# Kernel optimization log

Measured on AMD Instinct MI355X. Metric: run time of the kernel, lower is better.

## Reference

```python
import jax, jax.numpy as jnp
from jax import lax
import numpy as np

HEADS = 4
BUCKET = 64
DEPTH = 4


def _conv(x, w, b):
    y = lax.conv_general_dilated(x, w, (1, 1), [(1, 1), (1, 1)],
                                 dimension_numbers=('NCHW', 'OIHW', 'NCHW'))
    return y + b[None, :, None, None]


def _convT(x, w, b):
    # torch ConvTranspose2d(k=4, s=2, p=1): flip kernel, swap io, lhs_dilation=2, pad k-1-p=2
    wk = jnp.flip(w, (2, 3)).transpose(1, 0, 2, 3)
    y = lax.conv_general_dilated(x, wk, (1, 1), [(2, 2), (2, 2)], lhs_dilation=(2, 2),
                                 dimension_numbers=('NCHW', 'OIHW', 'NCHW'))
    return y + b[None, :, None, None]


def _maxpool(x):
    return lax.reduce_window(x, -jnp.inf, lax.max, (1, 1, 2, 2), (1, 1, 2, 2), 'VALID')


def _ln(x, g, b):
    m = x.mean(-1, keepdims=True)
    v = ((x - m) ** 2).mean(-1, keepdims=True)
    return (x - m) / jnp.sqrt(v + 1e-5) * g + b


def _lsh_attention(x, Wqk, bqk, Wv, bv, Wo, bo, rot):
    # shared-QK LSH bucketed attention (single hash round), look-one-back chunks
    B, N, D = x.shape
    h, dh = HEADS, D // HEADS
    qk = (x @ Wqk + bqk).reshape(B, N, h, dh).transpose(0, 2, 1, 3)  # B h N dh
    v = (x @ Wv + bv).reshape(B, N, h, dh).transpose(0, 2, 1, 3)
    k = qk / (jnp.linalg.norm(qk, axis=-1, keepdims=True) + 1e-6)    # keys = normalized queries
    rotated = jnp.einsum('bhnd,hdr->bhnr', qk, rot)
    buckets = jnp.argmax(jnp.concatenate([rotated, -rotated], -1), -1)  # B h N
    ticker = jnp.arange(N)
    perm = jnp.argsort(buckets * N + ticker, axis=-1)  # stable sort by bucket
    inv_perm = jnp.argsort(perm, axis=-1)
    g = lambda t: jnp.take_along_axis(t, perm[..., None], axis=2)
    nc = N // BUCKET
    bq = g(qk).reshape(B, h, nc, BUCKET, dh)
    bk = g(k).reshape(B, h, nc, BUCKET, dh)
    bv_ = g(v).reshape(B, h, nc, BUCKET, dh)
    bk2 = jnp.concatenate([bk, jnp.roll(bk, 1, axis=2)], axis=3)   # look one chunk back
    bv2 = jnp.concatenate([bv_, jnp.roll(bv_, 1, axis=2)], axis=3)
    dots = jnp.einsum('bhcid,bhcjd->bhcij', bq, bk2) * (dh ** -0.5)
    spos = jnp.take_along_axis(jnp.broadcast_to(ticker, buckets.shape), perm, -1).reshape(B, h, nc, BUCKET)
    kpos = jnp.concatenate([spos, jnp.roll(spos, 1, axis=2)], axis=3)
    dots = jnp.where(spos[..., :, None] == kpos[..., None, :], -1e5, dots)  # mask self (q == k)
    attn = jax.nn.softmax(dots, -1)
    o = jnp.einsum('bhcij,bhcjd->bhcid', attn, bv2).reshape(B, h, N, dh)
    o = jnp.take_along_axis(o, inv_perm[..., None], axis=2)  # unsort
    return o.transpose(0, 2, 1, 3).reshape(B, N, D) @ Wo + bo


def _reformer(seq, ln1_g, ln1_b, Wqk, bqk, Wv, bv, Wo, bo, rot, ln2_g, ln2_b, Wff1, bff1, Wff2, bff2):
    for i in range(DEPTH):
        seq = seq + _lsh_attention(_ln(seq, ln1_g[i], ln1_b[i]), Wqk[i], bqk[i], Wv[i], bv[i], Wo[i], bo[i], rot[i])
        hdn = jax.nn.gelu(_ln(seq, ln2_g[i], ln2_b[i]) @ Wff1[i] + bff1[i])
        seq = seq + hdn @ Wff2[i] + bff2[i]
    return seq


def _forward(burst, conv1_w, conv1_b, conv2_w, conv2_b, conv3_w, conv3_b,
             ln1_g, ln1_b, Wqk, bqk, Wv, bv, Wo, bo, rot, ln2_g, ln2_b,
             Wff1, bff1, Wff2, bff2, up1_w, up1_b, dec1_w, dec1_b,
             up2_w, up2_b, dec2_w, dec2_b, out_w, out_b):
    B, T, C, H, W = burst.shape
    x = burst.reshape(B * T, C, H, W)
    e1 = jax.nn.relu(_conv(x, conv1_w, conv1_b))
    p1 = _maxpool(e1)
    e2 = jax.nn.relu(_conv(p1, conv2_w, conv2_b))
    p2 = _maxpool(e2)
    bm = jax.nn.relu(_conv(p2, conv3_w, conv3_b))
    D = bm.shape[1]
    Hq, Wq = H // 4, W // 4
    seq = bm.transpose(0, 2, 3, 1).reshape(B * T, Hq * Wq, D)
    seq = _reformer(seq, ln1_g, ln1_b, Wqk, bqk, Wv, bv, Wo, bo, rot, ln2_g, ln2_b, Wff1, bff1, Wff2, bff2)
    bm = seq.reshape(B * T, Hq, Wq, D).transpose(0, 3, 1, 2)
    d1 = _convT(bm, up1_w, up1_b)
    d1 = jax.nn.relu(_conv(jnp.concatenate([d1, e2], 1), dec1_w, dec1_b))
    d2 = _convT(d1, up2_w, up2_b)
    d2 = jax.nn.relu(_conv(jnp.concatenate([d2, e1], 1), dec2_w, dec2_b))
    sharp = jax.nn.sigmoid(_conv(d2, out_w, out_b))
    return sharp.reshape(B, T, C, H, W)[:, 0]


def setup_inputs() -> dict:
    key = jax.random.key(0)
    ks = jax.random.split(key, 20)
    s = 0.05
    n = lambda k, shape: jax.random.normal(k, shape, jnp.float32) * s
    inp = {}
    inp['burst'] = jax.random.uniform(ks[0], (1, 7, 3, 256, 256), jnp.float32)
    inp['conv1_w'] = n(ks[1], (64, 3, 3, 3)); inp['conv1_b'] = jnp.zeros((64,), jnp.float32)
    inp['conv2_w'] = n(ks[2], (128, 64, 3, 3)); inp['conv2_b'] = jnp.zeros((128,), jnp.float32)
    inp['conv3_w'] = n(ks[3], (256, 128, 3, 3)); inp['conv3_b'] = jnp.zeros((256,), jnp.float32)
    inp['ln1_g'] = jnp.ones((4, 256), jnp.float32); inp['ln1_b'] = jnp.zeros((4, 256), jnp.float32)
    inp['Wqk'] = n(ks[4], (4, 256, 256)); inp['bqk'] = jnp.zeros((4, 256), jnp.float32)
    inp['Wv'] = n(ks[5], (4, 256, 256)); inp['bv'] = jnp.zeros((4, 256), jnp.float32)
    inp['Wo'] = n(ks[6], (4, 256, 256)); inp['bo'] = jnp.zeros((4, 256), jnp.float32)
    inp['rot'] = jax.random.normal(ks[7], (4, 4, 64, 32), jnp.float32)  # depth, heads, d_head, n_buckets//2
    inp['ln2_g'] = jnp.ones((4, 256), jnp.float32); inp['ln2_b'] = jnp.zeros((4, 256), jnp.float32)
    inp['Wff1'] = n(ks[8], (4, 256, 1024)); inp['bff1'] = jnp.zeros((4, 1024), jnp.float32)
    inp['Wff2'] = n(ks[9], (4, 1024, 256)); inp['bff2'] = jnp.zeros((4, 256), jnp.float32)
    inp['up1_w'] = n(ks[10], (256, 128, 4, 4)); inp['up1_b'] = jnp.zeros((128,), jnp.float32)
    inp['dec1_w'] = n(ks[11], (128, 256, 3, 3)); inp['dec1_b'] = jnp.zeros((128,), jnp.float32)
    inp['up2_w'] = n(ks[12], (128, 64, 4, 4)); inp['up2_b'] = jnp.zeros((64,), jnp.float32)
    inp['dec2_w'] = n(ks[13], (64, 128, 3, 3)); inp['dec2_b'] = jnp.zeros((64,), jnp.float32)
    inp['out_w'] = n(ks[14], (3, 64, 3, 3)); inp['out_b'] = jnp.zeros((3,), jnp.float32)
    return inp


def reference(burst, conv1_w, conv1_b, conv2_w, conv2_b, conv3_w, conv3_b,
              ln1_g, ln1_b, Wqk, bqk, Wv, bv, Wo, bo, rot, ln2_g, ln2_b,
              Wff1, bff1, Wff2, bff2, up1_w, up1_b, dec1_w, dec1_b,
              up2_w, up2_b, dec2_w, dec2_b, out_w, out_b):
    return _forward(burst, conv1_w, conv1_b, conv2_w, conv2_b, conv3_w, conv3_b,
                    ln1_g, ln1_b, Wqk, bqk, Wv, bv, Wo, bo, rot, ln2_g, ln2_b,
                    Wff1, bff1, Wff2, bff2, up1_w, up1_b, dec1_w, dec1_b,
                    up2_w, up2_b, dec2_w, dec2_b, out_w, out_b)
```

## Files before the change

kernel.cpp:

```cpp
#include <hip/hip_runtime.h>
#include <hip/hip_bf16.h>
#include <math.h>

using short8  = __attribute__((ext_vector_type(8))) short;
using half8   = __attribute__((ext_vector_type(8))) _Float16;
using floatx4 = __attribute__((ext_vector_type(4))) float;

static __device__ __forceinline__ float gelu_f(float x) {
    float x3 = x * x * x;
    return 0.5f * x * (1.f + tanhf(0.7978845608028654f * (x + 0.044715f * x3)));
}
static __device__ __forceinline__ short f2h(float f) {
    _Float16 h = (_Float16)f;
    return __builtin_bit_cast(short, h);
}
static __device__ __forceinline__ short f2bf(float f) {
    unsigned u = __float_as_uint(f);
    u += 0x7fffu + ((u >> 16) & 1u);
    return (short)(u >> 16);
}
static __device__ __forceinline__ float bf2f(short s) {
    return __uint_as_float(((unsigned)(unsigned short)s) << 16);
}
struct bf3s { short a, b, c; };
static __device__ __forceinline__ bf3s split3(float v) {
    short c0 = f2bf(v); float r = v - bf2f(c0);
    short c1 = f2bf(r); r -= bf2f(c1);
    short c2 = f2bf(r);
    bf3s s; s.a = c0; s.b = c1; s.c = c2; return s;
}

template <int OCB>
__global__ __launch_bounds__(256) void conv1_nhwc_kernel(
    const float* __restrict__ in1, const float* __restrict__ w,
    const float* __restrict__ bias, float* __restrict__ out, int H, int W, int OC)
{
    int tx = threadIdx.x, ty = threadIdx.y;
    int x = blockIdx.x * 16 + tx, y = blockIdx.y * 16 + ty;
    int oc0 = blockIdx.z * OCB;
    const int C = 3;
    float acc[OCB];
#pragma unroll
    for (int o = 0; o < OCB; ++o) acc[o] = 0.f;
    for (int ic = 0; ic < C; ++ic) {
        const float* src = in1 + (size_t)ic * H * W;
        float v[9];
#pragma unroll
        for (int ky = 0; ky < 3; ++ky) {
            int iy = y + ky - 1;
            bool okY = (iy >= 0) && (iy < H);
#pragma unroll
            for (int kx = 0; kx < 3; ++kx) {
                int ix = x + kx - 1;
                bool ok = okY && (ix >= 0) && (ix < W);
                v[ky * 3 + kx] = ok ? src[(size_t)iy * W + ix] : 0.f;
            }
        }
        const float* wp = w + ((size_t)oc0 * C + ic) * 9;
#pragma unroll
        for (int o = 0; o < OCB; ++o) {
            const float* wo = wp + (size_t)o * C * 9;
            acc[o] += v[0]*wo[0] + v[1]*wo[1] + v[2]*wo[2]
                    + v[3]*wo[3] + v[4]*wo[4] + v[5]*wo[5]
                    + v[6]*wo[6] + v[7]*wo[7] + v[8]*wo[8];
        }
    }
    float* op = out + ((size_t)y * W + x) * OC + oc0;
#pragma unroll
    for (int o = 0; o < OCB; ++o)
        op[o] = fmaxf(acc[o] + bias[oc0 + o], 0.f);
}

__global__ __launch_bounds__(256) void maxpool1_bf3_kernel(
    const float* __restrict__ in, short* __restrict__ o0, short* __restrict__ o1,
    short* __restrict__ o2, int OW, int IW, int C)
{
    int idx = blockIdx.x * 256 + threadIdx.x;
    int g = idx % (C >> 2); int p = idx / (C >> 2);
    int x = p % OW; int y = p / OW;
    size_t base = ((size_t)(2 * y) * IW + 2 * x) * C + g * 4;
    float4 a = *(const float4*)(in + base);
    float4 b = *(const float4*)(in + base + C);
    float4 c = *(const float4*)(in + base + (size_t)IW * C);
    float4 d = *(const float4*)(in + base + (size_t)IW * C + C);
    float v[4];
    v[0] = fmaxf(fmaxf(a.x, b.x), fmaxf(c.x, d.x));
    v[1] = fmaxf(fmaxf(a.y, b.y), fmaxf(c.y, d.y));
    v[2] = fmaxf(fmaxf(a.z, b.z), fmaxf(c.z, d.z));
    v[3] = fmaxf(fmaxf(a.w, b.w), fmaxf(c.w, d.w));
    size_t o = (size_t)p * C + g * 4;
#pragma unroll
    for (int j = 0; j < 4; ++j) {
        bf3s s = split3(v[j]);
        o0[o + j] = s.a; o1[o + j] = s.b; o2[o + j] = s.c;
    }
}

__global__ __launch_bounds__(256) void maxpool2_bf3_kernel(
    const short* __restrict__ i0, const short* __restrict__ i1,
    const short* __restrict__ i2, short* __restrict__ o0, short* __restrict__ o1,
    short* __restrict__ o2, int OW, int IW, int C)
{
    int idx = blockIdx.x * 256 + threadIdx.x;
    int g = idx % (C >> 2); int p = idx / (C >> 2);
    int x = p % OW; int y = p / OW;
    float v[4] = {-1e30f, -1e30f, -1e30f, -1e30f};
#pragma unroll
    for (int dy = 0; dy < 2; ++dy)
#pragma unroll
        for (int dx = 0; dx < 2; ++dx) {
            size_t base = ((size_t)(2 * y + dy) * IW + 2 * x + dx) * C + g * 4;
#pragma unroll
            for (int j = 0; j < 4; ++j) {
                float u = bf2f(i0[base + j]) + bf2f(i1[base + j]) + bf2f(i2[base + j]);
                v[j] = fmaxf(v[j], u);
            }
        }
    size_t o = (size_t)p * C + g * 4;
#pragma unroll
    for (int j = 0; j < 4; ++j) {
        bf3s s = split3(v[j]);
        o0[o + j] = s.a; o1[o + j] = s.b; o2[o + j] = s.c;
    }
}

__global__ void pack_conv3_kernel(const float* __restrict__ w,
                                  short* __restrict__ B0, short* __restrict__ B1,
                                  short* __restrict__ B2, int C, int OC, int total)
{
    int t = blockIdx.x * 256 + threadIdx.x;
    if (t >= total) return;
    int lane = t & 63, fi = t >> 6;
    int NT = OC >> 4;
    int nt = fi % NT, kt = fi / NT;
    int cpt = C >> 5;
    int tap = kt / cpt, ct = kt % cpt;
    int c = ct * 32 + (lane >> 4) * 8;
    int oc = nt * 16 + (lane & 15);
    short8 v0, v1, v2;
#pragma unroll
    for (int j = 0; j < 8; ++j) {
        bf3s s = split3(w[((size_t)oc * C + c + j) * 9 + tap]);
        v0[j] = s.a; v1[j] = s.b; v2[j] = s.c;
    }
    ((short8*)B0)[t] = v0; ((short8*)B1)[t] = v1; ((short8*)B2)[t] = v2;
}

__global__ __launch_bounds__(256) void conv_bf3_kernel(
    const short* __restrict__ ia0, const short* __restrict__ ia1,
    const short* __restrict__ ia2,
    const short* __restrict__ B0, const short* __restrict__ B1,
    const short* __restrict__ B2, const float* __restrict__ bias,
    float* __restrict__ outf, short* __restrict__ o0, short* __restrict__ o1,
    short* __restrict__ o2, short* __restrict__ oh,
    int H, int W, int C, int OC)
{
    int tid = threadIdx.x, wave = tid >> 6, lane = tid & 63;
    int quad = lane >> 4, l16 = lane & 15;
    int x0 = blockIdx.x * 64, y = blockIdx.y, nt0 = blockIdx.z * 4;
    int cpt = C >> 5, NT = OC >> 4;
    const short8* b0p = (const short8*)B0;
    const short8* b1p = (const short8*)B1;
    const short8* b2p = (const short8*)B2;
    floatx4 aM[4] = {{0,0,0,0},{0,0,0,0},{0,0,0,0},{0,0,0,0}};
    floatx4 aC[4] = {{0,0,0,0},{0,0,0,0},{0,0,0,0},{0,0,0,0}};
    int xm = x0 + wave * 16 + l16;
    for (int ky = 0; ky < 3; ++ky) {
        int yy = y + ky - 1;
        bool rok = (yy >= 0) && (yy < H);
        for (int kx = 0; kx < 3; ++kx) {
            int xx = xm + kx - 1;
            bool ok = rok && (xx >= 0) && (xx < W);
            size_t pos = (size_t)yy * W + xx;
            int ktb = (ky * 3 + kx) * cpt;
            for (int ct = 0; ct < cpt; ++ct) {
                int cc = ct * 32 + quad * 8;
                short8 A0 = {0,0,0,0,0,0,0,0}, A1 = A0, A2 = A0;
                if (ok) {
                    A0 = *(const short8*)(ia0 + pos * C + cc);
                    A1 = *(const short8*)(ia1 + pos * C + cc);
                    A2 = *(const short8*)(ia2 + pos * C + cc);
                }
                size_t bi = ((size_t)(ktb + ct) * NT + nt0) * 64 + lane;
#pragma unroll
                for (int s = 0; s < 4; ++s) {
                    short8 w0 = b0p[bi + s * 64];
                    short8 w1 = b1p[bi + s * 64];
                    short8 w2 = b2p[bi + s * 64];
                    aM[s] = __builtin_amdgcn_mfma_f32_16x16x32_bf16(A0, w0, aM[s], 0, 0, 0);
                    aC[s] = __builtin_amdgcn_mfma_f32_16x16x32_bf16(A0, w1, aC[s], 0, 0, 0);
                    aC[s] = __builtin_amdgcn_mfma_f32_16x16x32_bf16(A1, w0, aC[s], 0, 0, 0);
                    aC[s] = __builtin_amdgcn_mfma_f32_16x16x32_bf16(A0, w2, aC[s], 0, 0, 0);
                    aC[s] = __builtin_amdgcn_mfma_f32_16x16x32_bf16(A1, w1, aC[s], 0, 0, 0);
                    aC[s] = __builtin_amdgcn_mfma_f32_16x16x32_bf16(A2, w0, aC[s], 0, 0, 0);
                }
            }
        }
    }
#pragma unroll
    for (int s = 0; s < 4; ++s) {
        int n = (nt0 + s) * 16 + l16;
        float bs = bias[n];
#pragma unroll
        for (int r = 0; r < 4; ++r) {
            int m = wave * 16 + quad * 4 + r;
            int x = x0 + m;
            float v = fmaxf(aM[s][r] + aC[s][r] + bs, 0.f);
            size_t o = ((size_t)y * W + x) * OC + n;
            if (outf) outf[o] = v;
            else {
                bf3s sp = split3(v);
                o0[o] = sp.a; o1[o] = sp.b; o2[o] = sp.c;
                oh[o] = f2h(v);
            }
        }
    }
}

__global__ __launch_bounds__(256) void ln_bf3_kernel(
    const float* __restrict__ x, const float* __restrict__ g,
    const float* __restrict__ b, short* __restrict__ y0,
    short* __restrict__ y1, short* __restrict__ y2)
{
    int wave = threadIdx.x >> 6, lane = threadIdx.x & 63;
    int n = blockIdx.x * 4 + wave;
    const float* xr = x + (size_t)n * 256;
    float4 v = *(const float4*)(xr + lane * 4);
    float s = v.x + v.y + v.z + v.w;
#pragma unroll
    for (int m = 1; m < 64; m <<= 1) s += __shfl_xor(s, m);
    float mean = s * (1.f / 256.f);
    float cx = v.x - mean, cy = v.y - mean, cz = v.z - mean, cw = v.w - mean;
    float q = cx * cx + cy * cy + cz * cz + cw * cw;
#pragma unroll
    for (int m = 1; m < 64; m <<= 1) q += __shfl_xor(q, m);
    float rstd = rsqrtf(q * (1.f / 256.f) + 1e-5f);
    float4 gv = *(const float4*)(g + lane * 4);
    float4 bv = *(const float4*)(b + lane * 4);
    float o[4];
    o[0] = cx * rstd * gv.x + bv.x;
    o[1] = cy * rstd * gv.y + bv.y;
    o[2] = cz * rstd * gv.z + bv.z;
    o[3] = cw * rstd * gv.w + bv.w;
    size_t ob = (size_t)n * 256 + lane * 4;
#pragma unroll
    for (int j = 0; j < 4; ++j) {
        bf3s sp = split3(o[j]);
        y0[ob + j] = sp.a; y1[ob + j] = sp.b; y2[ob + j] = sp.c;
    }
}

__global__ __launch_bounds__(256) void knorm_kernel(
    const float* __restrict__ qk, float* __restrict__ knrm)
{
    int t = blockIdx.x * 256 + threadIdx.x;
    int h = t >> 12, n = t & 4095;
    const float* q = qk + (size_t)n * 256 + h * 64;
    float s = 0.f;
#pragma unroll
    for (int d = 0; d < 64; d += 4) {
        float4 v = *(const float4*)(q + d);
        s += v.x * v.x + v.y * v.y + v.z * v.z + v.w * v.w;
    }
    knrm[t] = 1.f / (sqrtf(s) + 1e-6f);
}

__global__ __launch_bounds__(256) void bucket_kernel(
    const float* __restrict__ qk, const float* __restrict__ rot,
    int* __restrict__ buckets)
{
    int t = blockIdx.x * 256 + threadIdx.x;
    int h = t >> 12, n = t & 4095;
    const float* q = qk + (size_t)n * 256 + h * 64;
    const float* R = rot + (size_t)h * 2048;
    float acc[32];
#pragma unroll
    for (int r = 0; r < 32; ++r) acc[r] = 0.f;
    for (int d = 0; d < 64; ++d) {
        float qd = q[d];
        const float* Rd = R + d * 32;
#pragma unroll
        for (int r = 0; r < 32; ++r) acc[r] += qd * Rd[r];
    }
    float bvv = acc[0]; int best = 0;
#pragma unroll
    for (int j = 1; j < 64; ++j) {
        float val = (j < 32) ? acc[j] : -acc[j - 32];
        if (val > bvv) { bvv = val; best = j; }
    }
    buckets[t] = best;
}

__global__ __launch_bounds__(256) void lsh_sort_kernel(
    const int* __restrict__ buckets, int* __restrict__ perm)
{
    int h = blockIdx.x;
    const int* bk = buckets + h * 4096;
    __shared__ unsigned long long mask[64][64];
    __shared__ int counts[64];
    __shared__ int offsets[64];
    __shared__ int wpre[64][64];
    int tid = threadIdx.x, wave = tid >> 6, lane = tid & 63;
    for (int w = wave * 16; w < wave * 16 + 16; ++w) {
        int bl = bk[w * 64 + lane];
        for (int b = 0; b < 64; ++b) {
            unsigned long long m = __ballot(bl == b);
            if (lane == b) mask[b][w] = m;
        }
    }
    __syncthreads();
    if (tid < 64) {
        int c = 0;
        for (int w = 0; w < 64; ++w) c += __popcll(mask[tid][w]);
        counts[tid] = c;
    }
    __syncthreads();
    if (tid == 0) {
        int a = 0;
        for (int b = 0; b < 64; ++b) { offsets[b] = a; a += counts[b]; }
    }
    __syncthreads();
    for (int b = wave * 16; b < wave * 16 + 16; ++b) {
        int c = __popcll(mask[b][lane]);
        int incl = c;
#pragma unroll
        for (int off = 1; off < 64; off <<= 1) {
            int nb = __shfl_up(incl, off);
            if (lane >= off) incl += nb;
        }
        wpre[b][lane] = incl - c + offsets[b];
    }
    __syncthreads();
    for (int i = tid; i < 4096; i += 256) {
        int b = bk[i]; int w = i >> 6; int l = i & 63;
        unsigned long long below = mask[b][w] & ((1ull << l) - 1ull);
        int pos = wpre[b][w] + __popcll(below);
        perm[h * 4096 + pos] = i;
    }
}

__global__ __launch_bounds__(256) void attn_kernel(
    const float* __restrict__ qk, const float* __restrict__ vv,
    const float* __restrict__ knrm, const int* __restrict__ perm,
    short* __restrict__ o0, short* __restrict__ o1, short* __restrict__ o2)
{
    __shared__ float ks[128 * 64];
    __shared__ float dotsT[128 * 64];
    int c = blockIdx.x, h = blockIdx.y;
    int tid = threadIdx.x;
    const int* pm = perm + h * 4096;
    int cm = (c + 63) & 63;
    {
        int jr = tid >> 1, hf = tid & 1;
        int sk = (jr < 64) ? (c * 64 + jr) : (cm * 64 + (jr - 64));
        int nk = pm[sk];
        float sc = knrm[h * 4096 + nk];
        const float* src = qk + (size_t)nk * 256 + h * 64 + hf * 32;
        float* dst = ks + jr * 64 + hf * 32;
#pragma unroll
        for (int d = 0; d < 32; d += 4) {
            float4 v = *(const float4*)(src + d);
            v.x *= sc; v.y *= sc; v.z *= sc; v.w *= sc;
            *(float4*)(dst + d) = v;
        }
    }
    __syncthreads();
    int r = tid & 63, jg = tid >> 6;
    int nq = pm[c * 64 + r];
    {
        float qreg[64];
        const float* src = qk + (size_t)nq * 256 + h * 64;
#pragma unroll
        for (int d = 0; d < 64; d += 4) {
            float4 v = *(const float4*)(src + d);
            qreg[d] = v.x; qreg[d + 1] = v.y; qreg[d + 2] = v.z; qreg[d + 3] = v.w;
        }
        for (int j = jg * 32; j < jg * 32 + 32; ++j) {
            const float* kr = ks + j * 64;
            float dot = 0.f;
#pragma unroll
            for (int d = 0; d < 64; ++d) dot += qreg[d] * kr[d];
            int sk = (j < 64) ? (c * 64 + j) : (cm * 64 + (j - 64));
            int nk = pm[sk];
            dot = (nk == nq) ? -1e5f : dot * 0.125f;
            dotsT[j * 64 + r] = dot;
        }
    }
    __syncthreads();
    {
        int jr = tid >> 1, hf = tid & 1;
        int sk = (jr < 64) ? (c * 64 + jr) : (cm * 64 + (jr - 64));
        int nk = pm[sk];
        const float* src = vv + (size_t)nk * 256 + h * 64 + hf * 32;
        float* dst = ks + jr * 64 + hf * 32;
#pragma unroll
        for (int d = 0; d < 32; d += 4)
            *(float4*)(dst + d) = *(const float4*)(src + d);
    }
    if (tid < 64) {
        int rr = tid;
        float mx = -1e30f;
        for (int j = 0; j < 128; ++j) mx = fmaxf(mx, dotsT[j * 64 + rr]);
        float s = 0.f;
        for (int j = 0; j < 128; ++j) {
            float e = expf(dotsT[j * 64 + rr] - mx);
            dotsT[j * 64 + rr] = e; s += e;
        }
        float inv = 1.f / s;
        for (int j = 0; j < 128; ++j) dotsT[j * 64 + rr] *= inv;
    }
    __syncthreads();
    int dg = jg;
    float acc[16];
#pragma unroll
    for (int d = 0; d < 16; ++d) acc[d] = 0.f;
    for (int j = 0; j < 128; ++j) {
        float a = dotsT[j * 64 + r];
        const float* vr = ks + j * 64 + dg * 16;
#pragma unroll
        for (int d = 0; d < 16; ++d) acc[d] += a * vr[d];
    }
    size_t ob = (size_t)nq * 256 + h * 64 + dg * 16;
#pragma unroll
    for (int d = 0; d < 16; ++d) {
        bf3s sp = split3(acc[d]);
        o0[ob + d] = sp.a; o1[ob + d] = sp.b; o2[ob + d] = sp.c;
    }
}

static __device__ __forceinline__ void pack_one(
    const float* __restrict__ W, short* __restrict__ B0, short* __restrict__ B1,
    short* __restrict__ B2, int N, int t)
{
    int lane = t & 63, fi = t >> 6;
    int NT = N >> 4;
    int nt = fi % NT, kt = fi / NT;
    int n = nt * 16 + (lane & 15);
    int k0 = kt * 32 + (lane >> 4) * 8;
    short8 v0, v1, v2;
#pragma unroll
    for (int j = 0; j < 8; ++j) {
        bf3s s = split3(W[(size_t)(k0 + j) * N + n]);
        v0[j] = s.a; v1[j] = s.b; v2[j] = s.c;
    }
    ((short8*)B0)[t] = v0; ((short8*)B1)[t] = v1; ((short8*)B2)[t] = v2;
}

__global__ void pack_layer_kernel(
    const float* __restrict__ Wqk, const float* __restrict__ Wv,
    const float* __restrict__ Wo, const float* __restrict__ Wff1,
    const float* __restrict__ Wff2,
    short* q0, short* q1, short* q2, short* v0, short* v1, short* v2,
    short* o0, short* o1, short* o2, short* f10, short* f11, short* f12,
    short* f20, short* f21, short* f22)
{
    int t = blockIdx.x * 256 + threadIdx.x;
    if (t < 8192)       pack_one(Wqk, q0, q1, q2, 256, t);
    else if (t < 16384) pack_one(Wv, v0, v1, v2, 256, t - 8192);
    else if (t < 24576) pack_one(Wo, o0, o1, o2, 256, t - 16384);
    else if (t < 57344) pack_one(Wff1, f10, f11, f12, 1024, t - 24576);
    else if (t < 90112) pack_one(Wff2, f20, f21, f22, 256, t - 57344);
}

static __device__ __forceinline__ void gemm_bf3_core(
    const short* __restrict__ A0, const short* __restrict__ A1,
    const short* __restrict__ A2,
    const short* __restrict__ B0, const short* __restrict__ B1,
    const short* __restrict__ B2, const float* __restrict__ bias,
    float* __restrict__ Cf, short* __restrict__ D0, short* __restrict__ D1,
    short* __restrict__ D2, int N, int K, int act, int resid, int bx, int by)
{
    int tid = threadIdx.x, wave = tid >> 6, lane = tid & 63;
    int quad = lane >> 4, l16 = lane & 15;
    int m0 = by * 64 + wave * 16;
    int NT = N >> 4, nt0 = bx * 4;
    size_t arow = (size_t)(m0 + l16) * K + quad * 8;
    const short8* b0p = (const short8*)B0;
    const short8* b1p = (const short8*)B1;
    const short8* b2p = (const short8*)B2;
    floatx4 aM[4] = {{0,0,0,0},{0,0,0,0},{0,0,0,0},{0,0,0,0}};
    floatx4 aC[4] = {{0,0,0,0},{0,0,0,0},{0,0,0,0},{0,0,0,0}};
    int KT = K >> 5;
    for (int kt = 0; kt < KT; ++kt) {
        short8 a0 = *(const short8*)(A0 + arow + kt * 32);
        short8 a1 = *(const short8*)(A1 + arow + kt * 32);
        short8 a2 = *(const short8*)(A2 + arow + kt * 32);
        size_t bi = ((size_t)kt * NT + nt0) * 64 + lane;
#pragma unroll
        for (int s = 0; s < 4; ++s) {
            short8 w0 = b0p[bi + s * 64];
            short8 w1 = b1p[bi + s * 64];
            short8 w2 = b2p[bi + s * 64];
            aM[s] = __builtin_amdgcn_mfma_f32_16x16x32_bf16(a0, w0, aM[s], 0, 0, 0);
            aC[s] = __builtin_amdgcn_mfma_f32_16x16x32_bf16(a0, w1, aC[s], 0, 0, 0);
            aC[s] = __builtin_amdgcn_mfma_f32_16x16x32_bf16(a1, w0, aC[s], 0, 0, 0);
            aC[s] = __builtin_amdgcn_mfma_f32_16x16x32_bf16(a0, w2, aC[s], 0, 0, 0);
            aC[s] = __builtin_amdgcn_mfma_f32_16x16x32_bf16(a1, w1, aC[s], 0, 0, 0);
            aC[s] = __builtin_amdgcn_mfma_f32_16x16x32_bf16(a2, w0, aC[s], 0, 0, 0);
        }
    }
#pragma unroll
    for (int s = 0; s < 4; ++s) {
        int n = (nt0 + s) * 16 + l16;
        float bs = bias[n];
#pragma unroll
        for (int r = 0; r < 4; ++r) {
            int m = m0 + quad * 4 + r;
            float v = aM[s][r] + aC[s][r] + bs;
            if (act == 1) v = gelu_f(v);
            size_t o = (size_t)m * N + n;
            if (D0) {
                bf3s sp = split3(v);
                D0[o] = sp.a; D1[o] = sp.b; D2[o] = sp.c;
            } else {
                if (resid) v += Cf[o];
                Cf[o] = v;
            }
        }
    }
}

__global__ __launch_bounds__(256) void gemm_bf3_kernel(
    const short* A0, const short* A1, const short* A2,
    const short* B0, const short* B1, const short* B2,
    const float* bias, float* Cf, short* D0, short* D1, short* D2,
    int N, int K, int act, int resid)
{
    gemm_bf3_core(A0, A1, A2, B0, B1, B2, bias, Cf, D0, D1, D2,
                  N, K, act, resid, blockIdx.x, blockIdx.y);
}

__global__ __launch_bounds__(256) void gemm_qkv_bf3_kernel(
    const short* A0, const short* A1, const short* A2,
    const short* Q0, const short* Q1, const short* Q2,
    const float* qb, float* Cq,
    const short* V0, const short* V1, const short* V2,
    const float* vb, float* Cv, int K)
{
    int side = blockIdx.x >> 2;
    gemm_bf3_core(A0, A1, A2, side ? V0 : Q0, side ? V1 : Q1, side ? V2 : Q2,
                  side ? vb : qb, side ? Cv : Cq, nullptr, nullptr, nullptr,
                  256, K, 0, 0, blockIdx.x & 3, blockIdx.y);
}

__global__ void pack_conv_kernel(const float* __restrict__ w, short* __restrict__ Bp,
                                 int C, int OC, int NT, int total)
{
    int t = blockIdx.x * 256 + threadIdx.x;
    if (t >= total) return;
    int lane = t & 63, fi = t >> 6;
    int nt = fi % NT, kt = fi / NT;
    int cpt = C >> 5;
    int tap = kt / cpt, ct = kt % cpt;
    int c = ct * 32 + (lane >> 4) * 8;
    int oc = nt * 16 + (lane & 15);
    short8 v;
#pragma unroll
    for (int j = 0; j < 8; ++j) {
        float f = (oc < OC) ? w[((size_t)oc * C + c + j) * 9 + tap] : 0.f;
        v[j] = f2h(f);
    }
    ((short8*)Bp)[t] = v;
}

__global__ void pack_convt_kernel(const float* __restrict__ w, short* __restrict__ Bp,
                                  int IC, int OC, int total)
{
    int t = blockIdx.x * 256 + threadIdx.x;
    if (t >= total) return;
    int lane = t & 63, fi = t >> 6;
    int NT = OC >> 4, cpt = IC >> 5, KT4 = 4 * cpt;
    int nt = fi % NT, r = fi / NT;
    int kt = r % KT4, pz = r / KT4;
    int py = pz >> 1, px = pz & 1;
    int t4 = kt / cpt, ct = kt % cpt;
    int ty = t4 >> 1, tx = t4 & 1;
    int ky = py ? (2 * ty) : (1 + 2 * ty);
    int kx = px ? (2 * tx) : (1 + 2 * tx);
    int ic = ct * 32 + (lane >> 4) * 8;
    int oc = nt * 16 + (lane & 15);
    short8 v;
#pragma unroll
    for (int j = 0; j < 8; ++j)
        v[j] = f2h(w[(((size_t)(ic + j) * OC + oc) * 4 + ky) * 4 + kx]);
    ((short8*)Bp)[t] = v;
}

__global__ __launch_bounds__(256) void conv_mfma_kernel(
    const short* __restrict__ in1, int C1, const short* __restrict__ in2, int C2,
    const short* __restrict__ Bp, const float* __restrict__ bias,
    short* __restrict__ outb, int H, int W, int OC)
{
    int tid = threadIdx.x, wave = tid >> 6, lane = tid & 63;
    int quad = lane >> 4, l16 = lane & 15;
    int x0 = blockIdx.x * 64, y = blockIdx.y, nt0 = blockIdx.z * 4;
    int C = C1 + C2, cpt = C >> 5, NT = OC >> 4;
    const half8* bp = (const half8*)Bp;
    floatx4 acc[4] = {{0,0,0,0},{0,0,0,0},{0,0,0,0},{0,0,0,0}};
    int xm = x0 + wave * 16 + l16;
    for (int ky = 0; ky < 3; ++ky) {
        int yy = y + ky - 1;
        bool rok = (yy >= 0) && (yy < H);
        for (int kx = 0; kx < 3; ++kx) {
            int xx = xm + kx - 1;
            bool ok = rok && (xx >= 0) && (xx < W);
            size_t pos = (size_t)yy * W + xx;
            int ktb = (ky * 3 + kx) * cpt;
            for (int ct = 0; ct < cpt; ++ct) {
                int cc = ct * 32 + quad * 8;
                half8 a = {};
                if (ok) {
                    const short* src = (cc < C1) ? (in1 + pos * C1 + cc)
                                                 : (in2 + pos * C2 + (cc - C1));
                    a = *(const half8*)src;
                }
                size_t bi = ((size_t)(ktb + ct) * NT + nt0) * 64 + lane;
#pragma unroll
                for (int s = 0; s < 4; ++s)
                    acc[s] = __builtin_amdgcn_mfma_f32_16x16x32_f16(a, bp[bi + s * 64], acc[s], 0, 0, 0);
            }
        }
    }
#pragma unroll
    for (int s = 0; s < 4; ++s) {
        int n = (nt0 + s) * 16 + l16;
        float bs = bias[n];
#pragma unroll
        for (int r = 0; r < 4; ++r) {
            int m = wave * 16 + quad * 4 + r;
            int x = x0 + m;
            float v = fmaxf(acc[s][r] + bs, 0.f);
            outb[((size_t)y * W + x) * OC + n] = f2h(v);
        }
    }
}

__global__ __launch_bounds__(256) void convt_mfma_kernel(
    const short* __restrict__ in, int IC, const short* __restrict__ Bp,
    const float* __restrict__ bias, short* __restrict__ outb, int IH, int IW, int OC)
{
    int tid = threadIdx.x, wave = tid >> 6, lane = tid & 63;
    int quad = lane >> 4, l16 = lane & 15;
    int pz = blockIdx.z & 3, nt0 = (blockIdx.z >> 2) * 4;
    int py = pz >> 1, px = pz & 1;
    int a0 = blockIdx.y, b0 = blockIdx.x * 64;
    int cpt = IC >> 5, NT = OC >> 4, KT4 = 4 * cpt;
    const half8* bp = (const half8*)Bp;
    floatx4 acc[4] = {{0,0,0,0},{0,0,0,0},{0,0,0,0},{0,0,0,0}};
    int bm = b0 + wave * 16 + l16;
    for (int ty = 0; ty < 2; ++ty) {
        int iy = a0 + (py ? (1 - ty) : (-ty));
        bool rok = (iy >= 0) && (iy < IH);
        for (int tx = 0; tx < 2; ++tx) {
            int ix = bm + (px ? (1 - tx) : (-tx));
            bool ok = rok && (ix >= 0) && (ix < IW);
            size_t pos = (size_t)iy * IW + ix;
            int ktb = (ty * 2 + tx) * cpt;
            for (int ct = 0; ct < cpt; ++ct) {
                int cc = ct * 32 + quad * 8;
                half8 a = {};
                if (ok) a = *(const half8*)(in + pos * IC + cc);
                size_t bi = ((size_t)(pz * KT4 + ktb + ct) * NT + nt0) * 64 + lane;
#pragma unroll
                for (int s = 0; s < 4; ++s)
                    acc[s] = __builtin_amdgcn_mfma_f32_16x16x32_f16(a, bp[bi + s * 64], acc[s], 0, 0, 0);
            }
        }
    }
    int OW = IW * 2;
    int oy = 2 * a0 + py;
#pragma unroll
    for (int s = 0; s < 4; ++s) {
        int n = (nt0 + s) * 16 + l16;
        float bs = bias[n];
#pragma unroll
        for (int r = 0; r < 4; ++r) {
            int m = wave * 16 + quad * 4 + r;
            int ox = 2 * (b0 + m) + px;
            outb[((size_t)oy * OW + ox) * OC + n] = f2h(acc[s][r] + bs);
        }
    }
}

__global__ __launch_bounds__(256) void convout_mfma_kernel(
    const short* __restrict__ in, const short* __restrict__ Bp,
    const float* __restrict__ bias, float* __restrict__ out, int H, int W)
{
    int tid = threadIdx.x, wave = tid >> 6, lane = tid & 63;
    int quad = lane >> 4, l16 = lane & 15;
    int x0 = blockIdx.x * 64, y = blockIdx.y;
    const int C = 64, cpt = 2;
    const half8* bp = (const half8*)Bp;
    floatx4 acc = {0,0,0,0};
    int xm = x0 + wave * 16 + l16;
    for (int ky = 0; ky < 3; ++ky) {
        int yy = y + ky - 1;
        bool rok = (yy >= 0) && (yy < H);
        for (int kx = 0; kx < 3; ++kx) {
            int xx = xm + kx - 1;
            bool ok = rok && (xx >= 0) && (xx < W);
            size_t pos = (size_t)yy * W + xx;
            int ktb = (ky * 3 + kx) * cpt;
#pragma unroll
            for (int ct = 0; ct < cpt; ++ct) {
                int cc = ct * 32 + quad * 8;
                half8 a = {};
                if (ok) a = *(const half8*)(in + pos * C + cc);
                acc = __builtin_amdgcn_mfma_f32_16x16x32_f16(
                          a, bp[(size_t)(ktb + ct) * 64 + lane], acc, 0, 0, 0);
            }
        }
    }
    int oc = l16;
    if (oc < 3) {
        float bs = bias[oc];
#pragma unroll
        for (int r = 0; r < 4; ++r) {
            int m = wave * 16 + quad * 4 + r;
            int x = x0 + m;
            float v = acc[r] + bs;
            out[(size_t)oc * H * W + (size_t)y * W + x] = 1.f / (1.f + expf(-v));
        }
    }
}

__global__ __launch_bounds__(256) void f2h_kernel(
    const float* __restrict__ in, short* __restrict__ out, int n)
{
    int i = blockIdx.x * 256 + threadIdx.x;
    if (i < n) out[i] = f2h(in[i]);
}

extern "C" void kernel_launch(void* const* d_in, const int* in_sizes, int n_in,
                              void* d_out, int out_size, void* d_ws, size_t ws_size,
                              hipStream_t stream)
{
    const float* burst   = (const float*)d_in[0];
    const float* conv1_w = (const float*)d_in[1];  const float* conv1_b = (const float*)d_in[2];
    const float* conv2_w = (const float*)d_in[3];  const float* conv2_b = (const float*)d_in[4];
    const float* conv3_w = (const float*)d_in[5];  const float* conv3_b = (const float*)d_in[6];
    const float* ln1_g   = (const float*)d_in[7];  const float* ln1_b   = (const float*)d_in[8];
    const float* Wqk     = (const float*)d_in[9];  const float* bqk     = (const float*)d_in[10];
    const float* Wv      = (const float*)d_in[11]; const float* bvv     = (const float*)d_in[12];
    const float* Wo      = (const float*)d_in[13]; const float* bo      = (const float*)d_in[14];
    const float* rot     = (const float*)d_in[15];
    const float* ln2_g   = (const float*)d_in[16]; const float* ln2_b   = (const float*)d_in[17];
    const float* Wff1    = (const float*)d_in[18]; const float* bff1    = (const float*)d_in[19];
    const float* Wff2    = (const float*)d_in[20]; const float* bff2    = (const float*)d_in[21];
    const float* up1_w   = (const float*)d_in[22]; const float* up1_b   = (const float*)d_in[23];
    const float* dec1_w  = (const float*)d_in[24]; const float* dec1_b  = (const float*)d_in[25];
    const float* up2_w   = (const float*)d_in[26]; const float* up2_b   = (const float*)d_in[27];
    const float* dec2_w  = (const float*)d_in[28]; const float* dec2_b  = (const float*)d_in[29];
    const float* out_w   = (const float*)d_in[30]; const float* out_b   = (const float*)d_in[31];

    float* ws = (float*)d_ws;
    short* e1h = (short*)(ws + 0);
    short* e2h = (short*)(ws + 2097152);
    float* seq = ws + 3145728;
    float* qkb = ws + 4194304;
    float* vvb = ws + 5242880;
    float* knb = ws + 6291456;
    int* buckets = (int*)(ws + 6307840);
    int* perm    = (int*)(ws + 6324224);
    short* xn0 = (short*)(ws + 6340608);
    short* xn1 = (short*)(ws + 6864896);
    short* xn2 = (short*)(ws + 7389184);
    short* hdn0 = (short*)(ws + 7913472);
    short* hdn1 = (short*)(ws + 10010624);
    short* hdn2 = (short*)(ws + 12107776);
    short* pqk0 = (short*)(ws + 14204928); short* pqk1 = (short*)(ws + 14237696); short* pqk2 = (short*)(ws + 14270464);
    short* pv0  = (short*)(ws + 14303232); short* pv1  = (short*)(ws + 14336000); short* pv2  = (short*)(ws + 14368768);
    short* po0  = (short*)(ws + 14401536); short* po1  = (short*)(ws + 14434304); short* po2  = (short*)(ws + 14467072);
    short* pf10 = (short*)(ws + 14499840); short* pf11 = (short*)(ws + 14630912); short* pf12 = (short*)(ws + 14761984);
    short* pf20 = (short*)(ws + 14893056); short* pf21 = (short*)(ws + 15024128); short* pf22 = (short*)(ws + 15155200);
    short* pdec1 = (short*)(ws + 15286272);
    short* pdec2 = (short*)(ws + 15433728);
    short* pout  = (short*)(ws + 15470592);
    short* pup1  = (short*)(ws + 15475200);
    short* pup2  = (short*)(ws + 15737344);
    float* e1f = ws + 7913472;
    short* p1_0 = (short*)(ws + 12107776); short* p1_1 = (short*)(ws + 12632064); short* p1_2 = (short*)(ws + 13156352);
    short* p2_0 = (short*)(ws + 13680640); short* p2_1 = (short*)(ws + 13942784); short* p2_2 = (short*)(ws + 14204928);
    short* pc2_0 = (short*)(ws + 14467072); short* pc2_1 = (short*)(ws + 14503936); short* pc2_2 = (short*)(ws + 14540800);
    short* pc3_0 = (short*)(ws + 14577664); short* pc3_1 = (short*)(ws + 14725120); short* pc3_2 = (short*)(ws + 14872576);
    short* e2_0 = (short*)(ws + 4194304); short* e2_1 = (short*)(ws + 5242880); short* e2_2 = (short*)(ws + 6291456);
    short* seqh = (short*)(ws + 7913472);
    short* d1   = (short*)(ws + 8437760);
    short* d1c  = (short*)(ws + 9486336);
    short* d2   = (short*)(ws + 10534912);
    short* d2c  = (short*)(ws + 12632064);

    dim3 b16(16, 16);

    pack_conv3_kernel<<<36, 256, 0, stream>>>(conv2_w, pc2_0, pc2_1, pc2_2, 64, 128, 9216);
    pack_conv3_kernel<<<144, 256, 0, stream>>>(conv3_w, pc3_0, pc3_1, pc3_2, 128, 256, 36864);
    pack_conv_kernel<<<144, 256, 0, stream>>>(dec1_w, pdec1, 256, 128, 8, 36864);
    pack_conv_kernel<<<36, 256, 0, stream>>>(dec2_w, pdec2, 128, 64, 4, 9216);
    pack_conv_kernel<<<5, 256, 0, stream>>>(out_w, pout, 64, 3, 1, 1152);
    pack_convt_kernel<<<256, 256, 0, stream>>>(up1_w, pup1, 256, 128, 65536);
    pack_convt_kernel<<<64, 256, 0, stream>>>(up2_w, pup2, 128, 64, 16384);

    conv1_nhwc_kernel<8><<<dim3(16, 16, 8), b16, 0, stream>>>(
        burst, conv1_w, conv1_b, e1f, 256, 256, 64);
    f2h_kernel<<<16384, 256, 0, stream>>>(e1f, e1h, 4194304);
    maxpool1_bf3_kernel<<<1024, 256, 0, stream>>>(e1f, p1_0, p1_1, p1_2, 128, 256, 64);
    conv_bf3_kernel<<<dim3(2, 128, 2), 256, 0, stream>>>(
        p1_0, p1_1, p1_2, pc2_0, pc2_1, pc2_2, conv2_b,
        nullptr, e2_0, e2_1, e2_2, e2h, 128, 128, 64, 128);
    maxpool2_bf3_kernel<<<512, 256, 0, stream>>>(
        e2_0, e2_1, e2_2, p2_0, p2_1, p2_2, 64, 128, 128);
    conv_bf3_kernel<<<dim3(1, 64, 4), 256, 0, stream>>>(
        p2_0, p2_1, p2_2, pc3_0, pc3_1, pc3_2, conv3_b,
        seq, nullptr, nullptr, nullptr, nullptr, 64, 64, 128, 256);

    for (int i = 0; i < 4; ++i) {
        pack_layer_kernel<<<352, 256, 0, stream>>>(
            Wqk + i * 65536, Wv + i * 65536, Wo + i * 65536,
            Wff1 + i * 262144, Wff2 + i * 262144,
            pqk0, pqk1, pqk2, pv0, pv1, pv2, po0, po1, po2,
            pf10, pf11, pf12, pf20, pf21, pf22);
        ln_bf3_kernel<<<1024, 256, 0, stream>>>(seq, ln1_g + i * 256, ln1_b + i * 256,
                                                xn0, xn1, xn2);
        gemm_qkv_bf3_kernel<<<dim3(8, 64), 256, 0, stream>>>(
            xn0, xn1, xn2, pqk0, pqk1, pqk2, bqk + i * 256, qkb,
            pv0, pv1, pv2, bvv + i * 256, vvb, 256);
        knorm_kernel<<<64, 256, 0, stream>>>(qkb, knb);
        bucket_kernel<<<64, 256, 0, stream>>>(qkb, rot + i * 8192, buckets);
        lsh_sort_kernel<<<4, 256, 0, stream>>>(buckets, perm);
        attn_kernel<<<dim3(64, 4), 256, 0, stream>>>(qkb, vvb, knb, perm, xn0, xn1, xn2);
        gemm_bf3_kernel<<<dim3(4, 64), 256, 0, stream>>>(
            xn0, xn1, xn2, po0, po1, po2, bo + i * 256, seq,
            nullptr, nullptr, nullptr, 256, 256, 0, 1);
        ln_bf3_kernel<<<1024, 256, 0, stream>>>(seq, ln2_g + i * 256, ln2_b + i * 256,
                                                xn0, xn1, xn2);
        gemm_bf3_kernel<<<dim3(16, 64), 256, 0, stream>>>(
            xn0, xn1, xn2, pf10, pf11, pf12, bff1 + i * 1024, nullptr,
            hdn0, hdn1, hdn2, 1024, 256, 1, 0);
        gemm_bf3_kernel<<<dim3(4, 64), 256, 0, stream>>>(
            hdn0, hdn1, hdn2, pf20, pf21, pf22, bff2 + i * 256, seq,
            nullptr, nullptr, nullptr, 256, 1024, 0, 1);
    }

    f2h_kernel<<<4096, 256, 0, stream>>>(seq, seqh, 1048576);
    convt_mfma_kernel<<<dim3(1, 64, 8), 256, 0, stream>>>(
        seqh, 256, pup1, up1_b, d1, 64, 64, 128);
    conv_mfma_kernel<<<dim3(2, 128, 2), 256, 0, stream>>>(
        d1, 128, e2h, 128, pdec1, dec1_b, d1c, 128, 128, 128);
    convt_mfma_kernel<<<dim3(2, 128, 4), 256, 0, stream>>>(
        d1c, 128, pup2, up2_b, d2, 128, 128, 64);
    conv_mfma_kernel<<<dim3(4, 256, 1), 256, 0, stream>>>(
        d2, 64, e1h, 64, pdec2, dec2_b, d2c, 256, 256, 64);
    convout_mfma_kernel<<<dim3(4, 256), 256, 0, stream>>>(
        d2c, pout, out_b, (float*)d_out, 256, 256);
}
```

Measured before the change: 1.367 ms.

## Prefetch GEMM operands, halve N-tile per block, fuse key norm into bucketing

The bf16x3 GEMM core now computes two 16-column tiles per wave instead of four, so grids double. It register-prefetches the next k-step's A and B fragments while issuing MFMAs on the current ones, and splits the correction accumulators into two chains to shorten dependency chains. The separate key-norm kernel is folded into the bucket kernel, which already reads each qk row, removing one launch and one pass over qk. Smaller tiles mean each A fragment is reused across fewer columns, raising A-load traffic in exchange for more blocks and better latency hiding.

After: 1.379 ms. About the same (+0.9%).

```diff
diff --git a/kernel.cpp b/kernel.cpp
--- a/kernel.cpp
+++ b/kernel.cpp
@@ -250,24 +250,9 @@
     }
 }
 
-__global__ __launch_bounds__(256) void knorm_kernel(
-    const float* __restrict__ qk, float* __restrict__ knrm)
-{
-    int t = blockIdx.x * 256 + threadIdx.x;
-    int h = t >> 12, n = t & 4095;
-    const float* q = qk + (size_t)n * 256 + h * 64;
-    float s = 0.f;
-#pragma unroll
-    for (int d = 0; d < 64; d += 4) {
-        float4 v = *(const float4*)(q + d);
-        s += v.x * v.x + v.y * v.y + v.z * v.z + v.w * v.w;
-    }
-    knrm[t] = 1.f / (sqrtf(s) + 1e-6f);
-}
-
-__global__ __launch_bounds__(256) void bucket_kernel(
+__global__ __launch_bounds__(256) void bucketn_kernel(
     const float* __restrict__ qk, const float* __restrict__ rot,
-    int* __restrict__ buckets)
+    int* __restrict__ buckets, float* __restrict__ knrm)
 {
     int t = blockIdx.x * 256 + threadIdx.x;
     int h = t >> 12, n = t & 4095;
@@ -276,12 +261,15 @@
     float acc[32];
 #pragma unroll
     for (int r = 0; r < 32; ++r) acc[r] = 0.f;
+    float s2 = 0.f;
     for (int d = 0; d < 64; ++d) {
         float qd = q[d];
+        s2 += qd * qd;
         const float* Rd = R + d * 32;
 #pragma unroll
         for (int r = 0; r < 32; ++r) acc[r] += qd * Rd[r];
     }
+    knrm[t] = 1.f / (sqrtf(s2) + 1e-6f);
     float bvv = acc[0]; int best = 0;
 #pragma unroll
     for (int j = 1; j < 64; ++j) {
@@ -473,40 +461,60 @@
     int tid = threadIdx.x, wave = tid >> 6, lane = tid & 63;
     int quad = lane >> 4, l16 = lane & 15;
     int m0 = by * 64 + wave * 16;
-    int NT = N >> 4, nt0 = bx * 4;
+    int NT = N >> 4, nt0 = bx * 2;
     size_t arow = (size_t)(m0 + l16) * K + quad * 8;
     const short8* b0p = (const short8*)B0;
     const short8* b1p = (const short8*)B1;
     const short8* b2p = (const short8*)B2;
-    floatx4 aM[4] = {{0,0,0,0},{0,0,0,0},{0,0,0,0},{0,0,0,0}};
-    floatx4 aC[4] = {{0,0,0,0},{0,0,0,0},{0,0,0,0},{0,0,0,0}};
+    floatx4 aM0 = {0,0,0,0}, aM1 = {0,0,0,0};
+    floatx4 aC10 = {0,0,0,0}, aC11 = {0,0,0,0};
+    floatx4 aC20 = {0,0,0,0}, aC21 = {0,0,0,0};
     int KT = K >> 5;
+    size_t bi0 = (size_t)nt0 * 64 + lane;
+    short8 a0 = *(const short8*)(A0 + arow);
+    short8 a1 = *(const short8*)(A1 + arow);
+    short8 a2 = *(const short8*)(A2 + arow);
+    short8 w00 = b0p[bi0], w01 = b1p[bi0], w02 = b2p[bi0];
+    short8 w10 = b0p[bi0 + 64], w11 = b1p[bi0 + 64], w12 = b2p[bi0 + 64];
     for (int kt = 0; kt < KT; ++kt) {
-        short8 a0 = *(const short8*)(A0 + arow + kt * 32);
-        short8 a1 = *(const short8*)(A1 + arow + kt * 32);
-        short8 a2 = *(const short8*)(A2 + arow + kt * 32);
-        size_t bi = ((size_t)kt * NT + nt0) * 64 + lane;
-#pragma unroll
-        for (int s = 0; s < 4; ++s) {
-            short8 w0 = b0p[bi + s * 64];
-            short8 w1 = b1p[bi + s * 64];
-            short8 w2 = b2p[bi + s * 64];
-            aM[s] = __builtin_amdgcn_mfma_f32_16x16x32_bf16(a0, w0, aM[s], 0, 0, 0);
-            aC[s] = __builtin_amdgcn_mfma_f32_16x16x32_bf16(a0, w1, aC[s], 0, 0, 0);
-            aC[s] = __builtin_amdgcn_mfma_f32_16x16x32_bf16(a1, w0, aC[s], 0, 0, 0);
-            aC[s] = __builtin_amdgcn_mfma_f32_16x16x32_bf16(a0, w2, aC[s], 0, 0, 0);
-            aC[s] = __builtin_amdgcn_mfma_f32_16x16x32_bf16(a1, w1, aC[s], 0, 0, 0);
-            aC[s] = __builtin_amdgcn_mfma_f32_16x16x32_bf16(a2, w0, aC[s], 0, 0, 0);
-        }
-    }
-#pragma unroll
-    for (int s = 0; s < 4; ++s) {
+        short8 na0 = {}, na1 = {}, na2 = {};
+        short8 nw00 = {}, nw01 = {}, nw02 = {}, nw10 = {}, nw11 = {}, nw12 = {};
+        if (kt + 1 < KT) {
+            size_t ar = arow + (size_t)(kt + 1) * 32;
+            na0 = *(const short8*)(A0 + ar);
+            na1 = *(const short8*)(A1 + ar);
+            na2 = *(const short8*)(A2 + ar);
+            size_t nbi = ((size_t)(kt + 1) * NT + nt0) * 64 + lane;
+            nw00 = b0p[nbi]; nw01 = b1p[nbi]; nw02 = b2p[nbi];
+            nw10 = b0p[nbi + 64]; nw11 = b1p[nbi + 64]; nw12 = b2p[nbi + 64];
+        }
+        aM0  = __builtin_amdgcn_mfma_f32_16x16x32_bf16(a0, w00, aM0, 0, 0, 0);
+        aM1  = __builtin_amdgcn_mfma_f32_16x16x32_bf16(a0, w10, aM1, 0, 0, 0);
+        aC10 = __builtin_amdgcn_mfma_f32_16x16x32_bf16(a0, w01, aC10, 0, 0, 0);
+        aC11 = __builtin_amdgcn_mfma_f32_16x16x32_bf16(a0, w11, aC11, 0, 0, 0);
+        aC20 = __builtin_amdgcn_mfma_f32_16x16x32_bf16(a1, w00, aC20, 0, 0, 0);
+        aC21 = __builtin_amdgcn_mfma_f32_16x16x32_bf16(a1, w10, aC21, 0, 0, 0);
+        aC10 = __builtin_amdgcn_mfma_f32_16x16x32_bf16(a0, w02, aC10, 0, 0, 0);
+        aC11 = __builtin_amdgcn_mfma_f32_16x16x32_bf16(a0, w12, aC11, 0, 0, 0);
+        aC20 = __builtin_amdgcn_mfma_f32_16x16x32_bf16(a1, w01, aC20, 0, 0, 0);
+        aC21 = __builtin_amdgcn_mfma_f32_16x16x32_bf16(a1, w11, aC21, 0, 0, 0);
+        aC10 = __builtin_amdgcn_mfma_f32_16x16x32_bf16(a2, w00, aC10, 0, 0, 0);
+        aC11 = __builtin_amdgcn_mfma_f32_16x16x32_bf16(a2, w10, aC11, 0, 0, 0);
+        a0 = na0; a1 = na1; a2 = na2;
+        w00 = nw00; w01 = nw01; w02 = nw02;
+        w10 = nw10; w11 = nw11; w12 = nw12;
+    }
+    floatx4 aM[2] = {aM0, aM1};
+    floatx4 c1[2] = {aC10, aC11};
+    floatx4 c2[2] = {aC20, aC21};
+#pragma unroll
+    for (int s = 0; s < 2; ++s) {
         int n = (nt0 + s) * 16 + l16;
         float bs = bias[n];
 #pragma unroll
         for (int r = 0; r < 4; ++r) {
             int m = m0 + quad * 4 + r;
-            float v = aM[s][r] + aC[s][r] + bs;
+            float v = aM[s][r] + (c1[s][r] + c2[s][r]) + bs;
             if (act == 1) v = gelu_f(v);
             size_t o = (size_t)m * N + n;
             if (D0) {
@@ -537,10 +545,10 @@
     const short* V0, const short* V1, const short* V2,
     const float* vb, float* Cv, int K)
 {
-    int side = blockIdx.x >> 2;
+    int side = blockIdx.x >> 3;
     gemm_bf3_core(A0, A1, A2, side ? V0 : Q0, side ? V1 : Q1, side ? V2 : Q2,
                   side ? vb : qb, side ? Cv : Cq, nullptr, nullptr, nullptr,
-                  256, K, 0, 0, blockIdx.x & 3, blockIdx.y);
+                  256, K, 0, 0, blockIdx.x & 7, blockIdx.y);
 }
 
 __global__ void pack_conv_kernel(const float* __restrict__ w, short* __restrict__ Bp,
@@ -821,22 +829,21 @@
             pf10, pf11, pf12, pf20, pf21, pf22);
         ln_bf3_kernel<<<1024, 256, 0, stream>>>(seq, ln1_g + i * 256, ln1_b + i * 256,
                                                 xn0, xn1, xn2);
-        gemm_qkv_bf3_kernel<<<dim3(8, 64), 256, 0, stream>>>(
+        gemm_qkv_bf3_kernel<<<dim3(16, 64), 256, 0, stream>>>(
             xn0, xn1, xn2, pqk0, pqk1, pqk2, bqk + i * 256, qkb,
             pv0, pv1, pv2, bvv + i * 256, vvb, 256);
-        knorm_kernel<<<64, 256, 0, stream>>>(qkb, knb);
-        bucket_kernel<<<64, 256, 0, stream>>>(qkb, rot + i * 8192, buckets);
+        bucketn_kernel<<<64, 256, 0, stream>>>(qkb, rot + i * 8192, buckets, knb);
         lsh_sort_kernel<<<4, 256, 0, stream>>>(buckets, perm);
         attn_kernel<<<dim3(64, 4), 256, 0, stream>>>(qkb, vvb, knb, perm, xn0, xn1, xn2);
-        gemm_bf3_kernel<<<dim3(4, 64), 256, 0, stream>>>(
+        gemm_bf3_kernel<<<dim3(8, 64), 256, 0, stream>>>(
             xn0, xn1, xn2, po0, po1, po2, bo + i * 256, seq,
             nullptr, nullptr, nullptr, 256, 256, 0, 1);
         ln_bf3_kernel<<<1024, 256, 0, stream>>>(seq, ln2_g + i * 256, ln2_b + i * 256,
                                                 xn0, xn1, xn2);
-        gemm_bf3_kernel<<<dim3(16, 64), 256, 0, stream>>>(
+        gemm_bf3_kernel<<<dim3(32, 64), 256, 0, stream>>>(
             xn0, xn1, xn2, pf10, pf11, pf12, bff1 + i * 1024, nullptr,
             hdn0, hdn1, hdn2, 1024, 256, 1, 0);
-        gemm_bf3_kernel<<<dim3(4, 64), 256, 0, stream>>>(
+        gemm_bf3_kernel<<<dim3(8, 64), 256, 0, stream>>>(
             hdn0, hdn1, hdn2, pf20, pf21, pf22, bff2 + i * 256, seq,
             nullptr, nullptr, nullptr, 256, 1024, 0, 1);
     }
```
